# Kernel optimization log

Measured on AMD Instinct MI355X. Metric: run time of the kernel, lower is better.

## Reference

```python
import jax, jax.numpy as jnp
import numpy as np

DELTA_V = 0.5
DELTA_D = 1.5
LOSS_WEIGHT = 1.0


def setup_inputs() -> dict:
    key = jax.random.key(0)
    k1, k2, k3, k4 = jax.random.split(key, 4)
    B, D, H, W = 8, 4, 640, 640
    return {
        "emb": jax.random.normal(k1, (B, D, H, W), dtype=jnp.float32),
        "instance": jax.random.randint(k2, (B, H, W), 0, 33, dtype=jnp.int32),
        "kernel": jax.random.uniform(k3, (B, H, W), dtype=jnp.float32),
        "training_mask": jax.random.uniform(k4, (B, H, W), dtype=jnp.float32),
        "num_labels": 33,  # static: background label 0 + 32 instances, all present w.h.p.
    }


def _single(emb, instance, kernel, tmask, num_labels):
    # emb: [D,H,W]; instance: [H,W] int; kernel/tmask: [H,W] float
    D = emb.shape[0]
    tm = (tmask > 0.5).astype(instance.dtype)
    kn = (kernel > 0.5).astype(instance.dtype)
    inst2 = instance * tm                      # instance masked by training mask
    inst_k = (inst2 * kn).reshape(-1)          # kernel-restricted labels, [N]
    inst = inst2.reshape(-1)                   # [N]
    x = emb.reshape(D, -1).T                   # [N, D]
    ones = jnp.ones(x.shape[0], jnp.float32)

    # per-instance kernel means (scatter-mean), label 0 column forced to zero
    sums = jax.ops.segment_sum(x, inst_k, num_segments=num_labels)      # [K1, D]
    cnts = jax.ops.segment_sum(ones, inst_k, num_segments=num_labels)   # [K1]
    mean = sums / jnp.maximum(cnts, 1.0)[:, None]
    mean = mean.at[0].set(0.0)

    # aggregation term: per-pixel distance to its instance mean, segmented mean over labels 1..K
    diff = x - mean[inst]                                               # [N, D]
    dist = jnp.sqrt(jnp.sum(diff * diff, axis=1))
    val = jnp.log(jnp.maximum(dist - DELTA_V, 0.0) ** 2 + 1.0)
    cnt_i = jax.ops.segment_sum(ones, inst, num_segments=num_labels)
    agg = jax.ops.segment_sum(val, inst, num_segments=num_labels) / jnp.maximum(cnt_i, 1.0)
    l_agg = jnp.mean(agg[1:])

    # discrimination term: pairwise distances between instance means (exclude label 0 and diagonal)
    m = mean[1:]                                                        # [K, D]
    K = m.shape[0]
    pdiff = m[:, None, :] - m[None, :, :]
    pd = jnp.sqrt(jnp.sum(pdiff * pdiff, axis=-1) + jnp.eye(K))         # diag padded (masked below)
    vald = jnp.log(jnp.maximum(2.0 * DELTA_D - pd, 0.0) ** 2 + 1.0)
    off = 1.0 - jnp.eye(K)
    l_dis = jnp.sum(vald * off) / (K * (K - 1))

    # regularizer: mean over all num_labels columns; label-0 column contributes log(1)=0
    nrm1 = jnp.sqrt(jnp.sum(m * m, axis=1))
    l_reg = jnp.sum(jnp.log(nrm1 + 1.0)) / num_labels * 0.001

    return l_agg + l_dis + l_reg


def reference(emb, instance, kernel, training_mask, num_labels):
    f = lambda e, i, k, t: _single(e, i, k, t, num_labels)
    loss_batch = jax.vmap(f)(emb, instance, kernel, training_mask)
    return jnp.mean(LOSS_WEIGHT * loss_batch)
```

## Files before the change

kernel.cpp:

```cpp
#include <hip/hip_runtime.h>
#include <math.h>

#define HW    409600
#define HW4   102400
#define BATCH 8
#define NLAB  33
#define WSF   231

__global__ void init_ws(float* ws) {
    int i = blockIdx.x * 256 + threadIdx.x;
    if (i < BATCH * WSF) ws[i] = 0.f;
}

__device__ __forceinline__ void acc1(int iv, float kv, float tv,
                                     float x0, float x1, float x2, float x3,
                                     float* bins) {
    int lab = (tv > 0.5f) ? iv : 0;
    if (lab != 0) {
        float* bb = bins + lab * 6;
        atomicAdd(bb + 5, 1.f);
        if (kv > 0.5f) {
            atomicAdd(bb + 0, x0);
            atomicAdd(bb + 1, x1);
            atomicAdd(bb + 2, x2);
            atomicAdd(bb + 3, x3);
            atomicAdd(bb + 4, 1.f);
        }
    }
}

__global__ __launch_bounds__(256) void pass1(const float* __restrict__ emb,
                                             const int*   __restrict__ inst,
                                             const float* __restrict__ kern,
                                             const float* __restrict__ tmask,
                                             float*       __restrict__ ws) {
    __shared__ float bins[4][NLAB * 6];
    int t = threadIdx.x, b = blockIdx.y, wave = t >> 6;
    for (int i = t; i < 4 * NLAB * 6; i += 256) (&bins[0][0])[i] = 0.f;
    __syncthreads();

    const float4* emb4  = (const float4*)(emb  + (size_t)b * 4 * HW);
    const int4*   inst4 = (const int4*)  (inst + (size_t)b * HW);
    const float4* kern4 = (const float4*)(kern + (size_t)b * HW);
    const float4* tm4   = (const float4*)(tmask+ (size_t)b * HW);
    float* mb = bins[wave];

    for (int p = blockIdx.x * 256 + t; p < HW4; p += gridDim.x * 256) {
        int4   iv = inst4[p];
        float4 kv = kern4[p];
        float4 tv = tm4[p];
        float4 x0 = emb4[p];
        float4 x1 = emb4[p + HW4];
        float4 x2 = emb4[p + 2 * HW4];
        float4 x3 = emb4[p + 3 * HW4];
        acc1(iv.x, kv.x, tv.x, x0.x, x1.x, x2.x, x3.x, mb);
        acc1(iv.y, kv.y, tv.y, x0.y, x1.y, x2.y, x3.y, mb);
        acc1(iv.z, kv.z, tv.z, x0.z, x1.z, x2.z, x3.z, mb);
        acc1(iv.w, kv.w, tv.w, x0.w, x1.w, x2.w, x3.w, mb);
    }
    __syncthreads();

    float* w = ws + b * WSF;
    for (int i = t; i < NLAB * 6; i += 256) {
        float v = bins[0][i] + bins[1][i] + bins[2][i] + bins[3][i];
        if (v != 0.f) {
            int lab = i / 6, f = i % 6;
            int dst = (f < 4) ? lab * 4 + f : (f == 4 ? 132 + lab : 165 + lab);
            atomicAdd(w + dst, v);
        }
    }
}

__global__ __launch_bounds__(256) void pass2(const float* __restrict__ emb,
                                             const int*   __restrict__ inst,
                                             const float* __restrict__ tmask,
                                             float*       __restrict__ ws) {
    __shared__ float mean_s[NLAB][4];
    __shared__ float vb[4][NLAB];
    int t = threadIdx.x, b = blockIdx.y, wave = t >> 6;
    float* w = ws + b * WSF;

    if (t < NLAB) {
        float inv = 1.f / fmaxf(w[132 + t], 1.f);
        float z = (t == 0) ? 0.f : 1.f;
        mean_s[t][0] = z * w[t * 4 + 0] * inv;
        mean_s[t][1] = z * w[t * 4 + 1] * inv;
        mean_s[t][2] = z * w[t * 4 + 2] * inv;
        mean_s[t][3] = z * w[t * 4 + 3] * inv;
    }
    for (int i = t; i < 4 * NLAB; i += 256) (&vb[0][0])[i] = 0.f;
    __syncthreads();

    const float4* emb4  = (const float4*)(emb  + (size_t)b * 4 * HW);
    const int4*   inst4 = (const int4*)  (inst + (size_t)b * HW);
    const float4* tm4   = (const float4*)(tmask+ (size_t)b * HW);
    float* mv = vb[wave];

    for (int p = blockIdx.x * 256 + t; p < HW4; p += gridDim.x * 256) {
        int4   iv = inst4[p];
        float4 tv = tm4[p];
        float4 x0 = emb4[p];
        float4 x1 = emb4[p + HW4];
        float4 x2 = emb4[p + 2 * HW4];
        float4 x3 = emb4[p + 3 * HW4];
        #pragma unroll
        for (int e = 0; e < 4; ++e) {
            int   ivv = (e == 0) ? iv.x : (e == 1) ? iv.y : (e == 2) ? iv.z : iv.w;
            float tvv = (e == 0) ? tv.x : (e == 1) ? tv.y : (e == 2) ? tv.z : tv.w;
            float a0  = (e == 0) ? x0.x : (e == 1) ? x0.y : (e == 2) ? x0.z : x0.w;
            float a1  = (e == 0) ? x1.x : (e == 1) ? x1.y : (e == 2) ? x1.z : x1.w;
            float a2  = (e == 0) ? x2.x : (e == 1) ? x2.y : (e == 2) ? x2.z : x2.w;
            float a3  = (e == 0) ? x3.x : (e == 1) ? x3.y : (e == 2) ? x3.z : x3.w;
            int lab = (tvv > 0.5f) ? ivv : 0;
            if (lab != 0) {
                float d0 = a0 - mean_s[lab][0];
                float d1 = a1 - mean_s[lab][1];
                float d2 = a2 - mean_s[lab][2];
                float d3 = a3 - mean_s[lab][3];
                float dist = sqrtf(d0 * d0 + d1 * d1 + d2 * d2 + d3 * d3);
                float u = fmaxf(dist - 0.5f, 0.f);
                atomicAdd(mv + lab, logf(u * u + 1.f));
            }
        }
    }
    __syncthreads();
    for (int i = t; i < NLAB; i += 256) {
        float v = vb[0][i] + vb[1][i] + vb[2][i] + vb[3][i];
        if (v != 0.f) atomicAdd(w + 198 + i, v);
    }
}

__global__ __launch_bounds__(256) void final_kernel(const float* __restrict__ ws,
                                                    float* __restrict__ out) {
    __shared__ float mean_s[NLAB][4];
    __shared__ float red[256];
    int t = threadIdx.x;
    float total = 0.f;
    for (int b = 0; b < BATCH; ++b) {
        const float* w = ws + b * WSF;
        if (t < NLAB) {
            float inv = 1.f / fmaxf(w[132 + t], 1.f);
            float z = (t == 0) ? 0.f : 1.f;
            mean_s[t][0] = z * w[t * 4 + 0] * inv;
            mean_s[t][1] = z * w[t * 4 + 1] * inv;
            mean_s[t][2] = z * w[t * 4 + 2] * inv;
            mean_s[t][3] = z * w[t * 4 + 3] * inv;
        }
        __syncthreads();
        float part = 0.f;
        if (t >= 1 && t < NLAB) {
            float ci = fmaxf(w[165 + t], 1.f);
            part = (w[198 + t] / ci) * (1.f / 32.f);
        }
        float disp = 0.f;
        for (int p = t; p < 1024; p += 256) {
            int i = p >> 5, j = p & 31;
            if (i != j) {
                float d0 = mean_s[i + 1][0] - mean_s[j + 1][0];
                float d1 = mean_s[i + 1][1] - mean_s[j + 1][1];
                float d2 = mean_s[i + 1][2] - mean_s[j + 1][2];
                float d3 = mean_s[i + 1][3] - mean_s[j + 1][3];
                float pd = sqrtf(d0 * d0 + d1 * d1 + d2 * d2 + d3 * d3);
                float u = fmaxf(2.0f * 1.5f - pd, 0.f);
                disp += logf(u * u + 1.f);
            }
        }
        disp *= 1.f / (32.f * 31.f);
        float regp = 0.f;
        if (t >= 1 && t < NLAB) {
            float n2 = mean_s[t][0] * mean_s[t][0] + mean_s[t][1] * mean_s[t][1] +
                       mean_s[t][2] * mean_s[t][2] + mean_s[t][3] * mean_s[t][3];
            regp = logf(sqrtf(n2) + 1.f) * (0.001f / 33.f);
        }
        red[t] = part + disp + regp;
        __syncthreads();
        for (int s = 128; s > 0; s >>= 1) {
            if (t < s) red[t] += red[t + s];
            __syncthreads();
        }
        if (t == 0) total += red[0];
        __syncthreads();
    }
    if (t == 0) out[0] = total * (1.f / BATCH);
}

extern "C" void kernel_launch(void* const* d_in, const int* in_sizes, int n_in,
                              void* d_out, int out_size, void* d_ws, size_t ws_size,
                              hipStream_t stream) {
    const float* emb   = (const float*)d_in[0];
    const int*   inst  = (const int*)  d_in[1];
    const float* kern  = (const float*)d_in[2];
    const float* tmask = (const float*)d_in[3];
    float* ws  = (float*)d_ws;
    float* out = (float*)d_out;

    init_ws<<<dim3((BATCH * WSF + 255) / 256), 256, 0, stream>>>(ws);
    dim3 grid(128, BATCH);
    pass1<<<grid, 256, 0, stream>>>(emb, inst, kern, tmask, ws);
    pass2<<<grid, 256, 0, stream>>>(emb, inst, tmask, ws);
    final_kernel<<<1, 256, 0, stream>>>(ws, out);
}
```

Measured before the change: 173.7 us.

## Pack masked labels to bytes, widen grid, and fold per-label normalization into pass2

Pass1 now writes a byte-packed masked label array to the workspace, so pass2 reads one uint per four pixels instead of the instance and training-mask arrays. The grid becomes 200 blocks per image with exactly two float4 groups per thread and no loop. Shared-memory histogram replicas go from 4 per wave to 8 per block to reduce atomic contention. Pass2 scales each pixel's term by the inverse label count and does a block tree reduction into one scalar, replacing per-label shared atomics, and fast __logf is used. This adds an extra global write of the label array and relies on the workspace being large enough, otherwise it falls back to recomputing labels.

```diff
diff --git a/kernel.cpp b/kernel.cpp
--- a/kernel.cpp
+++ b/kernel.cpp
@@ -5,21 +5,32 @@
 #define HW4   102400
 #define BATCH 8
 #define NLAB  33
-#define WSF   231
+#define GXB   200
+#define NREP  8
+#define RS    201
+#define WSB   208
+#define LAB_OFF 8192
+#define LAB_BYTES (4u * HW4 * BATCH)
 
 __global__ void init_ws(float* ws) {
     int i = blockIdx.x * 256 + threadIdx.x;
-    if (i < BATCH * WSF) ws[i] = 0.f;
-}
-
-__device__ __forceinline__ void acc1(int iv, float kv, float tv,
+    if (i < WSB * BATCH) ws[i] = 0.f;
+}
+
+__device__ __forceinline__ float getc(const float4& v, int e) {
+    return (e == 0) ? v.x : (e == 1) ? v.y : (e == 2) ? v.z : v.w;
+}
+__device__ __forceinline__ int geti(const int4& v, int e) {
+    return (e == 0) ? v.x : (e == 1) ? v.y : (e == 2) ? v.z : v.w;
+}
+
+__device__ __forceinline__ void acc1(int l, bool k,
                                      float x0, float x1, float x2, float x3,
-                                     float* bins) {
-    int lab = (tv > 0.5f) ? iv : 0;
-    if (lab != 0) {
-        float* bb = bins + lab * 6;
+                                     float* mb) {
+    if (l) {
+        float* bb = mb + l * 6;
         atomicAdd(bb + 5, 1.f);
-        if (kv > 0.5f) {
+        if (k) {
             atomicAdd(bb + 0, x0);
             atomicAdd(bb + 1, x1);
             atomicAdd(bb + 2, x2);
@@ -29,148 +40,192 @@
     }
 }
 
-__global__ __launch_bounds__(256) void pass1(const float* __restrict__ emb,
-                                             const int*   __restrict__ inst,
-                                             const float* __restrict__ kern,
-                                             const float* __restrict__ tmask,
-                                             float*       __restrict__ ws) {
-    __shared__ float bins[4][NLAB * 6];
-    int t = threadIdx.x, b = blockIdx.y, wave = t >> 6;
-    for (int i = t; i < 4 * NLAB * 6; i += 256) (&bins[0][0])[i] = 0.f;
-    __syncthreads();
-
-    const float4* emb4  = (const float4*)(emb  + (size_t)b * 4 * HW);
-    const int4*   inst4 = (const int4*)  (inst + (size_t)b * HW);
-    const float4* kern4 = (const float4*)(kern + (size_t)b * HW);
-    const float4* tm4   = (const float4*)(tmask+ (size_t)b * HW);
-    float* mb = bins[wave];
-
-    for (int p = blockIdx.x * 256 + t; p < HW4; p += gridDim.x * 256) {
-        int4   iv = inst4[p];
-        float4 kv = kern4[p];
-        float4 tv = tm4[p];
-        float4 x0 = emb4[p];
-        float4 x1 = emb4[p + HW4];
-        float4 x2 = emb4[p + 2 * HW4];
-        float4 x3 = emb4[p + 3 * HW4];
-        acc1(iv.x, kv.x, tv.x, x0.x, x1.x, x2.x, x3.x, mb);
-        acc1(iv.y, kv.y, tv.y, x0.y, x1.y, x2.y, x3.y, mb);
-        acc1(iv.z, kv.z, tv.z, x0.z, x1.z, x2.z, x3.z, mb);
-        acc1(iv.w, kv.w, tv.w, x0.w, x1.w, x2.w, x3.w, mb);
-    }
-    __syncthreads();
-
-    float* w = ws + b * WSF;
+__global__ __launch_bounds__(256, 4) void pass1(const float* __restrict__ emb,
+                                                const int*   __restrict__ inst,
+                                                const float* __restrict__ kern,
+                                                const float* __restrict__ tmask,
+                                                float*       __restrict__ ws,
+                                                unsigned*    __restrict__ labs) {
+    __shared__ float bins[NREP][RS];
+    const int t = threadIdx.x, bx = blockIdx.x, b = blockIdx.y;
+    float* mb = bins[(t >> 3) & (NREP - 1)];
+    for (int i = t; i < NREP * RS; i += 256) (&bins[0][0])[i] = 0.f;
+    __syncthreads();
+
+    const size_t  base  = (size_t)b * HW;
+    const float4* emb4  = (const float4*)(emb + base * 4);
+    const int4*   inst4 = (const int4*)(inst + base);
+    const float4* kern4 = (const float4*)(kern + base);
+    const float4* tm4   = (const float4*)(tmask + base);
+    const int gA = bx * 512 + t, gB = gA + 256;
+
+    int4   ivA = inst4[gA];          int4   ivB = inst4[gB];
+    float4 tvA = tm4[gA];            float4 tvB = tm4[gB];
+    float4 kvA = kern4[gA];          float4 kvB = kern4[gB];
+    float4 x0A = emb4[gA];           float4 x0B = emb4[gB];
+    float4 x1A = emb4[gA + HW4];     float4 x1B = emb4[gB + HW4];
+    float4 x2A = emb4[gA + 2*HW4];   float4 x2B = emb4[gB + 2*HW4];
+    float4 x3A = emb4[gA + 3*HW4];   float4 x3B = emb4[gB + 3*HW4];
+
+    int lA0 = (tvA.x > 0.5f) ? ivA.x : 0;
+    int lA1 = (tvA.y > 0.5f) ? ivA.y : 0;
+    int lA2 = (tvA.z > 0.5f) ? ivA.z : 0;
+    int lA3 = (tvA.w > 0.5f) ? ivA.w : 0;
+    int lB0 = (tvB.x > 0.5f) ? ivB.x : 0;
+    int lB1 = (tvB.y > 0.5f) ? ivB.y : 0;
+    int lB2 = (tvB.z > 0.5f) ? ivB.z : 0;
+    int lB3 = (tvB.w > 0.5f) ? ivB.w : 0;
+
+    if (labs) {
+        labs[(size_t)b * HW4 + gA] = (unsigned)lA0 | ((unsigned)lA1 << 8) |
+                                     ((unsigned)lA2 << 16) | ((unsigned)lA3 << 24);
+        labs[(size_t)b * HW4 + gB] = (unsigned)lB0 | ((unsigned)lB1 << 8) |
+                                     ((unsigned)lB2 << 16) | ((unsigned)lB3 << 24);
+    }
+
+    acc1(lA0, kvA.x > 0.5f, x0A.x, x1A.x, x2A.x, x3A.x, mb);
+    acc1(lA1, kvA.y > 0.5f, x0A.y, x1A.y, x2A.y, x3A.y, mb);
+    acc1(lA2, kvA.z > 0.5f, x0A.z, x1A.z, x2A.z, x3A.z, mb);
+    acc1(lA3, kvA.w > 0.5f, x0A.w, x1A.w, x2A.w, x3A.w, mb);
+    acc1(lB0, kvB.x > 0.5f, x0B.x, x1B.x, x2B.x, x3B.x, mb);
+    acc1(lB1, kvB.y > 0.5f, x0B.y, x1B.y, x2B.y, x3B.y, mb);
+    acc1(lB2, kvB.z > 0.5f, x0B.z, x1B.z, x2B.z, x3B.z, mb);
+    acc1(lB3, kvB.w > 0.5f, x0B.w, x1B.w, x2B.w, x3B.w, mb);
+    __syncthreads();
+
+    float* w = ws + b * WSB;
     for (int i = t; i < NLAB * 6; i += 256) {
-        float v = bins[0][i] + bins[1][i] + bins[2][i] + bins[3][i];
+        float v = 0.f;
+        #pragma unroll
+        for (int r = 0; r < NREP; ++r) v += bins[r][i];
         if (v != 0.f) {
             int lab = i / 6, f = i % 6;
-            int dst = (f < 4) ? lab * 4 + f : (f == 4 ? 132 + lab : 165 + lab);
+            int dst = (f < 4) ? lab * 4 + f : ((f == 4) ? 132 + lab : 165 + lab);
             atomicAdd(w + dst, v);
         }
     }
 }
 
-__global__ __launch_bounds__(256) void pass2(const float* __restrict__ emb,
-                                             const int*   __restrict__ inst,
-                                             const float* __restrict__ tmask,
-                                             float*       __restrict__ ws) {
-    __shared__ float mean_s[NLAB][4];
-    __shared__ float vb[4][NLAB];
-    int t = threadIdx.x, b = blockIdx.y, wave = t >> 6;
-    float* w = ws + b * WSF;
+template<bool USE_LABS>
+__global__ __launch_bounds__(256, 4) void pass2(const float* __restrict__ emb,
+                                                const int*   __restrict__ inst,
+                                                const float* __restrict__ tmask,
+                                                float*       __restrict__ ws,
+                                                const unsigned* __restrict__ labs) {
+    __shared__ float4 means4[NLAB];
+    __shared__ float  invci[NLAB];
+    __shared__ float  red[256];
+    const int t = threadIdx.x, bx = blockIdx.x, b = blockIdx.y;
+    float* w = ws + b * WSB;
 
     if (t < NLAB) {
         float inv = 1.f / fmaxf(w[132 + t], 1.f);
         float z = (t == 0) ? 0.f : 1.f;
-        mean_s[t][0] = z * w[t * 4 + 0] * inv;
-        mean_s[t][1] = z * w[t * 4 + 1] * inv;
-        mean_s[t][2] = z * w[t * 4 + 2] * inv;
-        mean_s[t][3] = z * w[t * 4 + 3] * inv;
-    }
-    for (int i = t; i < 4 * NLAB; i += 256) (&vb[0][0])[i] = 0.f;
-    __syncthreads();
-
-    const float4* emb4  = (const float4*)(emb  + (size_t)b * 4 * HW);
-    const int4*   inst4 = (const int4*)  (inst + (size_t)b * HW);
-    const float4* tm4   = (const float4*)(tmask+ (size_t)b * HW);
-    float* mv = vb[wave];
-
-    for (int p = blockIdx.x * 256 + t; p < HW4; p += gridDim.x * 256) {
-        int4   iv = inst4[p];
-        float4 tv = tm4[p];
-        float4 x0 = emb4[p];
-        float4 x1 = emb4[p + HW4];
-        float4 x2 = emb4[p + 2 * HW4];
-        float4 x3 = emb4[p + 3 * HW4];
-        #pragma unroll
-        for (int e = 0; e < 4; ++e) {
-            int   ivv = (e == 0) ? iv.x : (e == 1) ? iv.y : (e == 2) ? iv.z : iv.w;
-            float tvv = (e == 0) ? tv.x : (e == 1) ? tv.y : (e == 2) ? tv.z : tv.w;
-            float a0  = (e == 0) ? x0.x : (e == 1) ? x0.y : (e == 2) ? x0.z : x0.w;
-            float a1  = (e == 0) ? x1.x : (e == 1) ? x1.y : (e == 2) ? x1.z : x1.w;
-            float a2  = (e == 0) ? x2.x : (e == 1) ? x2.y : (e == 2) ? x2.z : x2.w;
-            float a3  = (e == 0) ? x3.x : (e == 1) ? x3.y : (e == 2) ? x3.z : x3.w;
-            int lab = (tvv > 0.5f) ? ivv : 0;
-            if (lab != 0) {
-                float d0 = a0 - mean_s[lab][0];
-                float d1 = a1 - mean_s[lab][1];
-                float d2 = a2 - mean_s[lab][2];
-                float d3 = a3 - mean_s[lab][3];
-                float dist = sqrtf(d0 * d0 + d1 * d1 + d2 * d2 + d3 * d3);
-                float u = fmaxf(dist - 0.5f, 0.f);
-                atomicAdd(mv + lab, logf(u * u + 1.f));
-            }
-        }
-    }
-    __syncthreads();
-    for (int i = t; i < NLAB; i += 256) {
-        float v = vb[0][i] + vb[1][i] + vb[2][i] + vb[3][i];
-        if (v != 0.f) atomicAdd(w + 198 + i, v);
-    }
+        means4[t] = make_float4(z * w[t * 4 + 0] * inv, z * w[t * 4 + 1] * inv,
+                                z * w[t * 4 + 2] * inv, z * w[t * 4 + 3] * inv);
+        invci[t] = 1.f / fmaxf(w[165 + t], 1.f);
+    }
+    __syncthreads();
+
+    const size_t  base = (size_t)b * HW;
+    const float4* emb4 = (const float4*)(emb + base * 4);
+    const int gA = bx * 512 + t, gB = gA + 256;
+
+    unsigned pkA, pkB;
+    if (USE_LABS) {
+        pkA = labs[(size_t)b * HW4 + gA];
+        pkB = labs[(size_t)b * HW4 + gB];
+    } else {
+        const int4*   inst4 = (const int4*)(inst + base);
+        const float4* tm4   = (const float4*)(tmask + base);
+        int4 ivA = inst4[gA], ivB = inst4[gB];
+        float4 tvA = tm4[gA], tvB = tm4[gB];
+        pkA = (unsigned)((tvA.x > 0.5f) ? ivA.x : 0)        |
+              ((unsigned)((tvA.y > 0.5f) ? ivA.y : 0) << 8) |
+              ((unsigned)((tvA.z > 0.5f) ? ivA.z : 0) << 16)|
+              ((unsigned)((tvA.w > 0.5f) ? ivA.w : 0) << 24);
+        pkB = (unsigned)((tvB.x > 0.5f) ? ivB.x : 0)        |
+              ((unsigned)((tvB.y > 0.5f) ? ivB.y : 0) << 8) |
+              ((unsigned)((tvB.z > 0.5f) ? ivB.z : 0) << 16)|
+              ((unsigned)((tvB.w > 0.5f) ? ivB.w : 0) << 24);
+    }
+
+    float4 x0A = emb4[gA];           float4 x0B = emb4[gB];
+    float4 x1A = emb4[gA + HW4];     float4 x1B = emb4[gB + HW4];
+    float4 x2A = emb4[gA + 2*HW4];   float4 x2B = emb4[gB + 2*HW4];
+    float4 x3A = emb4[gA + 3*HW4];   float4 x3B = emb4[gB + 3*HW4];
+
+    float acc = 0.f;
+    #pragma unroll
+    for (int e = 0; e < 4; ++e) {
+        int l = (pkA >> (8 * e)) & 255;
+        if (l) {
+            float4 m = means4[l];
+            float d0 = getc(x0A, e) - m.x, d1 = getc(x1A, e) - m.y;
+            float d2 = getc(x2A, e) - m.z, d3 = getc(x3A, e) - m.w;
+            float dist = sqrtf(d0 * d0 + d1 * d1 + d2 * d2 + d3 * d3);
+            float u = fmaxf(dist - 0.5f, 0.f);
+            acc += __logf(u * u + 1.f) * invci[l];
+        }
+    }
+    #pragma unroll
+    for (int e = 0; e < 4; ++e) {
+        int l = (pkB >> (8 * e)) & 255;
+        if (l) {
+            float4 m = means4[l];
+            float d0 = getc(x0B, e) - m.x, d1 = getc(x1B, e) - m.y;
+            float d2 = getc(x2B, e) - m.z, d3 = getc(x3B, e) - m.w;
+            float dist = sqrtf(d0 * d0 + d1 * d1 + d2 * d2 + d3 * d3);
+            float u = fmaxf(dist - 0.5f, 0.f);
+            acc += __logf(u * u + 1.f) * invci[l];
+        }
+    }
+
+    red[t] = acc;
+    __syncthreads();
+    for (int s = 128; s > 0; s >>= 1) {
+        if (t < s) red[t] += red[t + s];
+        __syncthreads();
+    }
+    if (t == 0) atomicAdd(w + 198, red[0]);
 }
 
 __global__ __launch_bounds__(256) void final_kernel(const float* __restrict__ ws,
                                                     float* __restrict__ out) {
-    __shared__ float mean_s[NLAB][4];
-    __shared__ float red[256];
+    __shared__ float4 means4[NLAB];
+    __shared__ float  red[256];
     int t = threadIdx.x;
     float total = 0.f;
     for (int b = 0; b < BATCH; ++b) {
-        const float* w = ws + b * WSF;
+        const float* w = ws + b * WSB;
+        __syncthreads();
         if (t < NLAB) {
             float inv = 1.f / fmaxf(w[132 + t], 1.f);
             float z = (t == 0) ? 0.f : 1.f;
-            mean_s[t][0] = z * w[t * 4 + 0] * inv;
-            mean_s[t][1] = z * w[t * 4 + 1] * inv;
-            mean_s[t][2] = z * w[t * 4 + 2] * inv;
-            mean_s[t][3] = z * w[t * 4 + 3] * inv;
+            means4[t] = make_float4(z * w[t * 4 + 0] * inv, z * w[t * 4 + 1] * inv,
+                                    z * w[t * 4 + 2] * inv, z * w[t * 4 + 3] * inv);
         }
         __syncthreads();
         float part = 0.f;
-        if (t >= 1 && t < NLAB) {
-            float ci = fmaxf(w[165 + t], 1.f);
-            part = (w[198 + t] / ci) * (1.f / 32.f);
-        }
+        if (t == 0) part = w[198] * (1.f / 32.f);
         float disp = 0.f;
         for (int p = t; p < 1024; p += 256) {
             int i = p >> 5, j = p & 31;
             if (i != j) {
-                float d0 = mean_s[i + 1][0] - mean_s[j + 1][0];
-                float d1 = mean_s[i + 1][1] - mean_s[j + 1][1];
-                float d2 = mean_s[i + 1][2] - mean_s[j + 1][2];
-                float d3 = mean_s[i + 1][3] - mean_s[j + 1][3];
+                float4 mi = means4[i + 1], mj = means4[j + 1];
+                float d0 = mi.x - mj.x, d1 = mi.y - mj.y;
+                float d2 = mi.z - mj.z, d3 = mi.w - mj.w;
                 float pd = sqrtf(d0 * d0 + d1 * d1 + d2 * d2 + d3 * d3);
-                float u = fmaxf(2.0f * 1.5f - pd, 0.f);
-                disp += logf(u * u + 1.f);
+                float u = fmaxf(3.0f - pd, 0.f);
+                disp += __logf(u * u + 1.f);
             }
         }
-        disp *= 1.f / (32.f * 31.f);
+        disp *= 1.f / 992.f;
         float regp = 0.f;
         if (t >= 1 && t < NLAB) {
-            float n2 = mean_s[t][0] * mean_s[t][0] + mean_s[t][1] * mean_s[t][1] +
-                       mean_s[t][2] * mean_s[t][2] + mean_s[t][3] * mean_s[t][3];
-            regp = logf(sqrtf(n2) + 1.f) * (0.001f / 33.f);
+            float4 m = means4[t];
+            float n2 = m.x * m.x + m.y * m.y + m.z * m.z + m.w * m.w;
+            regp = __logf(sqrtf(n2) + 1.f) * (0.001f / 33.f);
         }
         red[t] = part + disp + regp;
         __syncthreads();
@@ -179,7 +234,6 @@
             __syncthreads();
         }
         if (t == 0) total += red[0];
-        __syncthreads();
     }
     if (t == 0) out[0] = total * (1.f / BATCH);
 }
@@ -194,9 +248,13 @@
     float* ws  = (float*)d_ws;
     float* out = (float*)d_out;
 
-    init_ws<<<dim3((BATCH * WSF + 255) / 256), 256, 0, stream>>>(ws);
-    dim3 grid(128, BATCH);
-    pass1<<<grid, 256, 0, stream>>>(emb, inst, kern, tmask, ws);
-    pass2<<<grid, 256, 0, stream>>>(emb, inst, tmask, ws);
+    const bool use_labs = ws_size >= (size_t)LAB_OFF + LAB_BYTES;
+    unsigned* labs = use_labs ? (unsigned*)((char*)d_ws + LAB_OFF) : nullptr;
+
+    init_ws<<<dim3((WSB * BATCH + 255) / 256), 256, 0, stream>>>(ws);
+    dim3 grid(GXB, BATCH);
+    pass1<<<grid, 256, 0, stream>>>(emb, inst, kern, tmask, ws, labs);
+    if (use_labs) pass2<true ><<<grid, 256, 0, stream>>>(emb, inst, tmask, ws, labs);
+    else          pass2<false><<<grid, 256, 0, stream>>>(emb, inst, tmask, ws, nullptr);
     final_kernel<<<1, 256, 0, stream>>>(ws, out);
 }
```

Result: no change. 173.3 us (-0.2%).
